# Kernel tuning notes

Measured on AMD Instinct MI355X. Metric: run time of the kernel, lower is better.

## Reference

```python
import jax, jax.numpy as jnp
import numpy as np

WINDOW = (2, 6, 12)  # (Wz, Wh, Ww), N = 144
HEADS = 6
TYPE_OF_WINDOWS = 10


def _position_index(ws):
    Wz, Wh, Ww = ws
    zi = np.arange(Wz); zj = -np.arange(Wz) * Wz
    hi = np.arange(Wh); hj = -np.arange(Wh) * Wh
    w = np.arange(Ww)
    c1 = np.stack(np.meshgrid(zi, hi, w, indexing='ij')).reshape(3, -1)
    c2 = np.stack(np.meshgrid(zj, hj, w, indexing='ij')).reshape(3, -1)
    coords = (c1[:, :, None] - c2[:, None, :]).transpose(1, 2, 0).copy()
    coords[:, :, 2] += Ww - 1
    coords[:, :, 1] *= 2 * Ww - 1
    coords[:, :, 0] *= (2 * Ww - 1) * Wh * Wh
    return coords.sum(-1).reshape(-1)  # [N*N]


def setup_inputs() -> dict:
    key = jax.random.key(0)
    ks = jax.random.split(key, 7)
    B, nW, C = 96, TYPE_OF_WINDOWS, 192
    N = WINDOW[0] * WINDOW[1] * WINDOW[2]
    bias_len = (2 * WINDOW[2] - 1) * WINDOW[1] ** 2 * WINDOW[0] ** 2
    return {
        'x': jax.random.normal(ks[0], (B, nW, N, C), jnp.float32),
        'mask': jax.random.normal(ks[1], (B, N, N), jnp.float32),
        'w_qkv': jax.random.normal(ks[2], (C, 3 * C), jnp.float32) * 0.02,
        'b_qkv': jnp.zeros((3 * C,), jnp.float32),
        'w_proj': jax.random.normal(ks[3], (C, C), jnp.float32) * 0.02,
        'b_proj': jnp.zeros((C,), jnp.float32),
        'bias_table': jax.random.normal(ks[4], (bias_len, nW, HEADS), jnp.float32) * 0.02,
        'position_index': jnp.asarray(_position_index(WINDOW), jnp.int32),
    }


def reference(x, mask, w_qkv, b_qkv, w_proj, b_proj, bias_table, position_index):
    B, nW, N, C = x.shape
    H = HEADS
    Dh = C // H
    scale = Dh ** -0.5
    qkv = x @ w_qkv + b_qkv                       # [B,nW,N,3C]
    qkv = qkv.reshape(B, nW, N, 3, H, Dh)
    qkv = qkv.transpose(3, 0, 1, 4, 2, 5)         # [3,B,nW,H,N,Dh]
    q, k, v = qkv[0], qkv[1], qkv[2]
    attn = jnp.einsum('bwhnd,bwhmd->bwhnm', q * scale, k)   # [B,nW,H,N,N]
    bias = bias_table[position_index]             # [N*N,nW,H]
    bias = bias.reshape(N, N, nW, H).transpose(2, 3, 0, 1)  # [nW,H,N,N]
    attn = attn + bias[None] + mask[:, None, None, :, :]
    attn = jax.nn.softmax(attn, axis=-1)
    out = jnp.einsum('bwhnm,bwhmd->bwhnd', attn, v)         # [B,nW,H,N,Dh]
    out = out.transpose(0, 1, 3, 2, 4).reshape(B, nW, N, C)
    return out @ w_proj + b_proj
```

## Files before the change

kernel.cpp:

```cpp
#include <hip/hip_runtime.h>
#include <math.h>

#define B_   96
#define NW   10
#define NN   144
#define CC   192
#define HH   6
#define DH   32
#define SCALE 0.17677669529663687f

#define XP 200
#define PP 152
#define NPASS 3
#define BWCHUNK 320
#define QKV_STRIDE (NN * DH)

typedef __attribute__((ext_vector_type(8))) short v8s;
typedef __attribute__((ext_vector_type(4))) unsigned short v4us;
typedef __attribute__((ext_vector_type(4))) float v4f;

__device__ __forceinline__ unsigned short f2b(float f) {
  union { float f; unsigned u; } v; v.f = f;
  unsigned r = v.u + 0x7fffu + ((v.u >> 16) & 1u);
  return (unsigned short)(r >> 16);
}
__device__ __forceinline__ float b2f(unsigned short s) {
  union { unsigned u; float f; } v; v.u = ((unsigned)s) << 16;
  return v.f;
}

#define N_WQT (576*192)
#define N_WPT (192*192)
#define N_BIAS (NW*HH*NN*NN)

__global__ __launch_bounds__(256) void prep_kernel(
    const float* __restrict__ w_qkv, const float* __restrict__ w_proj,
    const float* __restrict__ bias_table, const int* __restrict__ pos,
    unsigned short* __restrict__ wqT, unsigned short* __restrict__ wpT,
    unsigned short* __restrict__ biasNN)
{
  int i = blockIdx.x * 256 + threadIdx.x;
  if (i < N_WQT) {
    int n = i / 192, k = i % 192;
    wqT[i] = f2b(w_qkv[k * 576 + n]);
  } else if (i < N_WQT + N_WPT) {
    int j = i - N_WQT;
    int n = j / 192, k = j % 192;
    wpT[j] = f2b(w_proj[k * 192 + n]);
  } else if (i < N_WQT + N_WPT + N_BIAS) {
    int j = i - (N_WQT + N_WPT);
    int m = j % NN, n = (j / NN) % NN, h = (j / (NN * NN)) % HH, w = j / (NN * NN * HH);
    biasNN[j] = f2b(bias_table[(pos[n * NN + m] * NW + w) * HH + h]);
  }
}

__global__ __launch_bounds__(256, 3) void qkv_gemm(
    const float* __restrict__ x, const float* __restrict__ b_qkv,
    const unsigned short* __restrict__ wqT,
    unsigned short* __restrict__ qkv, int bw0)
{
  __shared__ unsigned short xs[48 * XP];
  const int tid  = threadIdx.x;
  const int wave = tid >> 6, lane = tid & 63;
  const int lr = lane & 15, lk8 = (lane >> 4) * 8, quad = lane >> 4;
  const int bwl = blockIdx.x / 3;
  const int rt3 = blockIdx.x % 3;
  const int bw  = bw0 + bwl;

  const float4* xp4 = (const float4*)(x + ((size_t)bw * NN + rt3 * 48) * CC);
  for (int i = tid; i < 48 * (CC / 4); i += 256) {
    float4 f = xp4[i];
    int r = i / (CC / 4), c = (i % (CC / 4)) * 4;
    unsigned short* d = &xs[r * XP + c];
    d[0] = f2b(f.x); d[1] = f2b(f.y); d[2] = f2b(f.z); d[3] = f2b(f.w);
  }
  __syncthreads();

  v8s a[3][6];
  #pragma unroll
  for (int ii = 0; ii < 3; ii++)
    #pragma unroll
    for (int ks = 0; ks < 6; ks++)
      a[ii][ks] = *(const v8s*)&xs[(ii * 16 + lr) * XP + ks * 32 + lk8];

  for (int c = wave; c < 36; c += 4) {
    const int s = c / 12;
    const int h = (c % 12) >> 1;
    const int dhalf = c & 1;
    const unsigned short* wrow = wqT + (size_t)(c * 16 + lr) * CC;
    v8s bf[6];
    #pragma unroll
    for (int ks = 0; ks < 6; ks++) bf[ks] = *(const v8s*)&wrow[ks * 32 + lk8];
    const float bv = b_qkv[c * 16 + lr];
    v4f acc[3];
    #pragma unroll
    for (int ii = 0; ii < 3; ii++) acc[ii] = (v4f){bv, bv, bv, bv};
    #pragma unroll
    for (int ks = 0; ks < 6; ks++)
      #pragma unroll
      for (int ii = 0; ii < 3; ii++)
        acc[ii] = __builtin_amdgcn_mfma_f32_16x16x32_bf16(a[ii][ks], bf[ks], acc[ii], 0, 0, 0);

    if (s == 2) {
      unsigned short* opT = qkv + ((size_t)(bwl * HH + h) * 3 + 2) * QKV_STRIDE
                          + (size_t)(dhalf * 16 + lr) * NN;
      #pragma unroll
      for (int ii = 0; ii < 3; ii++) {
        const int n0 = rt3 * 48 + ii * 16 + quad * 4;
        v4us pk;
        #pragma unroll
        for (int r = 0; r < 4; r++) pk[r] = f2b(acc[ii][r]);
        *(v4us*)&opT[n0] = pk;
      }
    } else {
      unsigned short* op = qkv + ((size_t)(bwl * HH + h) * 3 + s) * QKV_STRIDE + dhalf * 16 + lr;
      #pragma unroll
      for (int ii = 0; ii < 3; ii++)
        #pragma unroll
        for (int r = 0; r < 4; r++) {
          const int n = rt3 * 48 + ii * 16 + quad * 4 + r;
          op[n * DH] = f2b(acc[ii][r]);
        }
    }
  }
}

__global__ __launch_bounds__(256, 2) void attn_bwh(
    const unsigned short* __restrict__ qkv, const float* __restrict__ mask,
    const unsigned short* __restrict__ biasNN,
    unsigned short* __restrict__ ao, int bw0)
{
  __shared__ unsigned short Ps[NN * PP];

  const int tid  = threadIdx.x;
  const int wave = tid >> 6, lane = tid & 63;
  const int lr = lane & 15, lk8 = (lane >> 4) * 8, quad = lane >> 4;

  const int bwl = blockIdx.x / HH;
  const int h   = blockIdx.x % HH;
  const int bw  = bw0 + bwl;
  const int b   = bw / NW;
  const int w   = bw % NW;

  const unsigned short* qp = qkv + (size_t)(bwl * HH + h) * 3 * QKV_STRIDE;
  const unsigned short* kp = qp + QKV_STRIDE;
  const unsigned short* vT = qp + 2 * QKV_STRIDE;

  v8s bv[2][4], bvt[2];
  #pragma unroll
  for (int dh2 = 0; dh2 < 2; dh2++) {
    const unsigned short* vrow = vT + (size_t)(dh2 * 16 + lr) * NN;
    #pragma unroll
    for (int ks = 0; ks < 4; ks++) bv[dh2][ks] = *(const v8s*)&vrow[ks * 32 + lk8];
    bvt[dh2] = *(const v8s*)&vrow[128 + (lk8 & 8)];
  }

  v8s aq[9];
  #pragma unroll
  for (int nt = 0; nt < 9; nt++)
    aq[nt] = *(const v8s*)&qp[(nt * 16 + lr) * DH + lk8];

  for (int mt = wave; mt < 9; mt += 4) {
    v8s bk = *(const v8s*)&kp[(mt * 16 + lr) * DH + lk8];
    const int m = mt * 16 + lr;
    #pragma unroll
    for (int nt = 0; nt < 9; nt++) {
      v4f c = {0.f, 0.f, 0.f, 0.f};
      c = __builtin_amdgcn_mfma_f32_16x16x32_bf16(aq[nt], bk, c, 0, 0, 0);
      #pragma unroll
      for (int r = 0; r < 4; r++) {
        const int n = nt * 16 + quad * 4 + r;
        Ps[n * PP + m] = f2b(c[r] * SCALE);
      }
    }
  }
  __syncthreads();

  const unsigned short* bp = biasNN + (size_t)(w * HH + h) * NN * NN;
  const float* mp = mask + (size_t)b * NN * NN;
  for (int rr = 0; rr < 9; rr++) {
    const int row = rr * 16 + wave * 4 + quad;
    unsigned short* prow = &Ps[row * PP];
    const unsigned short* brow = bp + (size_t)row * NN;
    const float* mrow = mp + (size_t)row * NN;
    float bm[9];
    #pragma unroll
    for (int j = 0; j < 9; j++)
      bm[j] = b2f(brow[j * 16 + lr]) + mrow[j * 16 + lr];
    float e[9];
    float mx = -1e30f;
    #pragma unroll
    for (int j = 0; j < 9; j++) {
      e[j] = b2f(prow[j * 16 + lr]) + bm[j];
      mx = fmaxf(mx, e[j]);
    }
    #pragma unroll
    for (int off = 8; off; off >>= 1) mx = fmaxf(mx, __shfl_xor(mx, off, 64));
    float s = 0.f;
    #pragma unroll
    for (int j = 0; j < 9; j++) { e[j] = __expf(e[j] - mx); s += e[j]; }
    #pragma unroll
    for (int off = 8; off; off >>= 1) s += __shfl_xor(s, off, 64);
    const float inv = 1.f / s;
    #pragma unroll
    for (int j = 0; j < 9; j++) prow[j * 16 + lr] = f2b(e[j] * inv);
  }
  __syncthreads();

  const v8s vzero = {};
  for (int nt = wave; nt < 9; nt += 4) {
    v8s ap[4];
    #pragma unroll
    for (int ks = 0; ks < 4; ks++)
      ap[ks] = *(const v8s*)&Ps[(nt * 16 + lr) * PP + ks * 32 + lk8];
    v8s at = *(const v8s*)&Ps[(nt * 16 + lr) * PP + 128 + (lk8 & 8)];
    at = (quad < 2) ? at : vzero;
    #pragma unroll
    for (int dh2 = 0; dh2 < 2; dh2++) {
      v4f c = {0.f, 0.f, 0.f, 0.f};
      #pragma unroll
      for (int ks = 0; ks < 4; ks++)
        c = __builtin_amdgcn_mfma_f32_16x16x32_bf16(ap[ks], bv[dh2][ks], c, 0, 0, 0);
      c = __builtin_amdgcn_mfma_f32_16x16x32_bf16(at, bvt[dh2], c, 0, 0, 0);
      #pragma unroll
      for (int r = 0; r < 4; r++) {
        const int n = nt * 16 + quad * 4 + r;
        ao[((size_t)bw * NN + n) * CC + h * DH + dh2 * 16 + lr] = f2b(c[r]);
      }
    }
  }
}

__global__ __launch_bounds__(256) void proj_mfma(
    const unsigned short* __restrict__ ao,
    const unsigned short* __restrict__ wpT,
    const float* __restrict__ b_proj,
    float* __restrict__ out)
{
  const int tid  = threadIdx.x;
  const int wave = tid >> 6, lane = tid & 63;
  const int lr = lane & 15, lk8 = (lane >> 4) * 8, quad = lane >> 4;
  const size_t row0 = (size_t)blockIdx.x * 64;
  const int j0 = wave * 3;

  v8s bf[3][6];
  #pragma unroll
  for (int jj = 0; jj < 3; jj++)
    #pragma unroll
    for (int ks = 0; ks < 6; ks++)
      bf[jj][ks] = *(const v8s*)(wpT + (size_t)((j0 + jj) * 16 + lr) * CC + ks * 32 + lk8);

  float bvj[3];
  #pragma unroll
  for (int jj = 0; jj < 3; jj++) bvj[jj] = b_proj[(j0 + jj) * 16 + lr];

  #pragma unroll
  for (int rt = 0; rt < 4; rt++) {
    const size_t r0 = row0 + rt * 16;
    v8s a[6];
    #pragma unroll
    for (int ks = 0; ks < 6; ks++)
      a[ks] = *(const v8s*)(ao + (r0 + lr) * CC + ks * 32 + lk8);
    v4f acc[3];
    #pragma unroll
    for (int jj = 0; jj < 3; jj++) acc[jj] = (v4f){bvj[jj], bvj[jj], bvj[jj], bvj[jj]};
    #pragma unroll
    for (int ks = 0; ks < 6; ks++)
      #pragma unroll
      for (int jj = 0; jj < 3; jj++)
        acc[jj] = __builtin_amdgcn_mfma_f32_16x16x32_bf16(a[ks], bf[jj][ks], acc[jj], 0, 0, 0);
    #pragma unroll
    for (int jj = 0; jj < 3; jj++)
      #pragma unroll
      for (int r = 0; r < 4; r++)
        out[(r0 + quad * 4 + r) * CC + (j0 + jj) * 16 + lr] = acc[jj][r];
  }
}

extern "C" void kernel_launch(void* const* d_in, const int* in_sizes, int n_in,
                              void* d_out, int out_size, void* d_ws, size_t ws_size,
                              hipStream_t stream)
{
  const float* x          = (const float*)d_in[0];
  const float* mask       = (const float*)d_in[1];
  const float* w_qkv      = (const float*)d_in[2];
  const float* b_qkv      = (const float*)d_in[3];
  const float* w_proj     = (const float*)d_in[4];
  const float* b_proj     = (const float*)d_in[5];
  const float* bias_table = (const float*)d_in[6];
  const int*   pos        = (const int*)d_in[7];
  float* out = (float*)d_out;

  unsigned short* biasNN = (unsigned short*)d_ws;
  unsigned short* wqT    = biasNN + N_BIAS;
  unsigned short* wpT    = wqT + N_WQT;
  unsigned short* qkvws  = wpT + N_WPT;
  unsigned short* ao     = qkvws + (size_t)BWCHUNK * HH * 3 * QKV_STRIDE;

  const int prep_total = N_WQT + N_WPT + N_BIAS;
  prep_kernel<<<(prep_total + 255) / 256, 256, 0, stream>>>(
      w_qkv, w_proj, bias_table, pos, wqT, wpT, biasNN);

  for (int p = 0; p < NPASS; p++) {
    const int bw0 = p * BWCHUNK;
    qkv_gemm<<<BWCHUNK * 3, 256, 0, stream>>>(x, b_qkv, wqT, qkvws, bw0);
    attn_bwh<<<BWCHUNK * HH, 256, 0, stream>>>(qkvws, mask, biasNN, ao, bw0);
  }
  proj_mfma<<<(B_ * NW * NN) / 64, 256, 0, stream>>>(ao, wpT, b_proj, out);
}
```

Measured before the change: 476.1 us.

## Fuse QKV projection into attention kernel with per-head LDS staging

```diff
diff --git a/kernel.cpp b/kernel.cpp
--- a/kernel.cpp
+++ b/kernel.cpp
@@ -9,11 +9,10 @@
 #define DH   32
 #define SCALE 0.17677669529663687f
 
-#define XP 200
+#define QP 40
+#define TP 168
 #define PP 152
-#define NPASS 3
-#define BWCHUNK 320
-#define QKV_STRIDE (NN * DH)
+#define NBW (B_ * NW)
 
 typedef __attribute__((ext_vector_type(8))) short v8s;
 typedef __attribute__((ext_vector_type(4))) unsigned short v4us;
@@ -32,14 +31,24 @@
 #define N_WQT (576*192)
 #define N_WPT (192*192)
 #define N_BIAS (NW*HH*NN*NN)
+#define N_X4  (B_*NW*NN*CC/4)
 
 __global__ __launch_bounds__(256) void prep_kernel(
     const float* __restrict__ w_qkv, const float* __restrict__ w_proj,
     const float* __restrict__ bias_table, const int* __restrict__ pos,
+    const float* __restrict__ x,
     unsigned short* __restrict__ wqT, unsigned short* __restrict__ wpT,
-    unsigned short* __restrict__ biasNN)
+    unsigned short* __restrict__ biasNN, unsigned short* __restrict__ xb)
 {
   int i = blockIdx.x * 256 + threadIdx.x;
+  if (i < N_X4) {
+    float4 f = ((const float4*)x)[i];
+    v4us pk;
+    pk[0] = f2b(f.x); pk[1] = f2b(f.y); pk[2] = f2b(f.z); pk[3] = f2b(f.w);
+    *(v4us*)&xb[i * 4] = pk;
+    return;
+  }
+  i -= N_X4;
   if (i < N_WQT) {
     int n = i / 192, k = i % 192;
     wqT[i] = f2b(w_qkv[k * 576 + n]);
@@ -54,102 +63,62 @@
   }
 }
 
-__global__ __launch_bounds__(256, 3) void qkv_gemm(
-    const float* __restrict__ x, const float* __restrict__ b_qkv,
-    const unsigned short* __restrict__ wqT,
-    unsigned short* __restrict__ qkv, int bw0)
-{
-  __shared__ unsigned short xs[48 * XP];
+__global__ __launch_bounds__(256, 2) void fused_attn(
+    const unsigned short* __restrict__ xb, const float* __restrict__ b_qkv,
+    const unsigned short* __restrict__ wqT, const float* __restrict__ mask,
+    const unsigned short* __restrict__ biasNN,
+    unsigned short* __restrict__ ao)
+{
+  __shared__ unsigned short q_lds[NN * QP];
+  __shared__ unsigned short k_lds[NN * QP];
+  __shared__ unsigned short vT[DH * TP];
+  __shared__ unsigned short Ps[NN * PP];
+
   const int tid  = threadIdx.x;
   const int wave = tid >> 6, lane = tid & 63;
   const int lr = lane & 15, lk8 = (lane >> 4) * 8, quad = lane >> 4;
-  const int bwl = blockIdx.x / 3;
-  const int rt3 = blockIdx.x % 3;
-  const int bw  = bw0 + bwl;
-
-  const float4* xp4 = (const float4*)(x + ((size_t)bw * NN + rt3 * 48) * CC);
-  for (int i = tid; i < 48 * (CC / 4); i += 256) {
-    float4 f = xp4[i];
-    int r = i / (CC / 4), c = (i % (CC / 4)) * 4;
-    unsigned short* d = &xs[r * XP + c];
-    d[0] = f2b(f.x); d[1] = f2b(f.y); d[2] = f2b(f.z); d[3] = f2b(f.w);
+
+  const int bw = blockIdx.x / HH;
+  const int h  = blockIdx.x % HH;
+  const int b  = bw / NW;
+  const int w  = bw % NW;
+
+  const unsigned short* xrow = xb + (size_t)bw * NN * CC;
+  for (int t = wave; t < 54; t += 4) {
+    const int nt = t / 6, c = t % 6;
+    const int s = c >> 1, dhalf = c & 1;
+    const int cg = s * 12 + h * 2 + dhalf;
+    v8s a_[6], bf_[6];
+    #pragma unroll
+    for (int ks = 0; ks < 6; ks++)
+      a_[ks] = *(const v8s*)&xrow[(nt * 16 + lr) * CC + ks * 32 + lk8];
+    #pragma unroll
+    for (int ks = 0; ks < 6; ks++)
+      bf_[ks] = *(const v8s*)&wqT[(size_t)(cg * 16 + lr) * CC + ks * 32 + lk8];
+    const float bv0 = b_qkv[cg * 16 + lr];
+    v4f acc = {bv0, bv0, bv0, bv0};
+    #pragma unroll
+    for (int ks = 0; ks < 6; ks++)
+      acc = __builtin_amdgcn_mfma_f32_16x16x32_bf16(a_[ks], bf_[ks], acc, 0, 0, 0);
+    const int d = dhalf * 16 + lr;
+    if (s == 2) {
+      v4us pk;
+      #pragma unroll
+      for (int r = 0; r < 4; r++) pk[r] = f2b(acc[r]);
+      *(v4us*)&vT[d * TP + nt * 16 + quad * 4] = pk;
+    } else {
+      unsigned short* dst = (s == 0) ? q_lds : k_lds;
+      #pragma unroll
+      for (int r = 0; r < 4; r++)
+        dst[(nt * 16 + quad * 4 + r) * QP + d] = f2b(acc[r]);
+    }
   }
   __syncthreads();
 
-  v8s a[3][6];
-  #pragma unroll
-  for (int ii = 0; ii < 3; ii++)
-    #pragma unroll
-    for (int ks = 0; ks < 6; ks++)
-      a[ii][ks] = *(const v8s*)&xs[(ii * 16 + lr) * XP + ks * 32 + lk8];
-
-  for (int c = wave; c < 36; c += 4) {
-    const int s = c / 12;
-    const int h = (c % 12) >> 1;
-    const int dhalf = c & 1;
-    const unsigned short* wrow = wqT + (size_t)(c * 16 + lr) * CC;
-    v8s bf[6];
-    #pragma unroll
-    for (int ks = 0; ks < 6; ks++) bf[ks] = *(const v8s*)&wrow[ks * 32 + lk8];
-    const float bv = b_qkv[c * 16 + lr];
-    v4f acc[3];
-    #pragma unroll
-    for (int ii = 0; ii < 3; ii++) acc[ii] = (v4f){bv, bv, bv, bv};
-    #pragma unroll
-    for (int ks = 0; ks < 6; ks++)
-      #pragma unroll
-      for (int ii = 0; ii < 3; ii++)
-        acc[ii] = __builtin_amdgcn_mfma_f32_16x16x32_bf16(a[ii][ks], bf[ks], acc[ii], 0, 0, 0);
-
-    if (s == 2) {
-      unsigned short* opT = qkv + ((size_t)(bwl * HH + h) * 3 + 2) * QKV_STRIDE
-                          + (size_t)(dhalf * 16 + lr) * NN;
-      #pragma unroll
-      for (int ii = 0; ii < 3; ii++) {
-        const int n0 = rt3 * 48 + ii * 16 + quad * 4;
-        v4us pk;
-        #pragma unroll
-        for (int r = 0; r < 4; r++) pk[r] = f2b(acc[ii][r]);
-        *(v4us*)&opT[n0] = pk;
-      }
-    } else {
-      unsigned short* op = qkv + ((size_t)(bwl * HH + h) * 3 + s) * QKV_STRIDE + dhalf * 16 + lr;
-      #pragma unroll
-      for (int ii = 0; ii < 3; ii++)
-        #pragma unroll
-        for (int r = 0; r < 4; r++) {
-          const int n = rt3 * 48 + ii * 16 + quad * 4 + r;
-          op[n * DH] = f2b(acc[ii][r]);
-        }
-    }
-  }
-}
-
-__global__ __launch_bounds__(256, 2) void attn_bwh(
-    const unsigned short* __restrict__ qkv, const float* __restrict__ mask,
-    const unsigned short* __restrict__ biasNN,
-    unsigned short* __restrict__ ao, int bw0)
-{
-  __shared__ unsigned short Ps[NN * PP];
-
-  const int tid  = threadIdx.x;
-  const int wave = tid >> 6, lane = tid & 63;
-  const int lr = lane & 15, lk8 = (lane >> 4) * 8, quad = lane >> 4;
-
-  const int bwl = blockIdx.x / HH;
-  const int h   = blockIdx.x % HH;
-  const int bw  = bw0 + bwl;
-  const int b   = bw / NW;
-  const int w   = bw % NW;
-
-  const unsigned short* qp = qkv + (size_t)(bwl * HH + h) * 3 * QKV_STRIDE;
-  const unsigned short* kp = qp + QKV_STRIDE;
-  const unsigned short* vT = qp + 2 * QKV_STRIDE;
-
   v8s bv[2][4], bvt[2];
   #pragma unroll
   for (int dh2 = 0; dh2 < 2; dh2++) {
-    const unsigned short* vrow = vT + (size_t)(dh2 * 16 + lr) * NN;
+    const unsigned short* vrow = &vT[(dh2 * 16 + lr) * TP];
     #pragma unroll
     for (int ks = 0; ks < 4; ks++) bv[dh2][ks] = *(const v8s*)&vrow[ks * 32 + lk8];
     bvt[dh2] = *(const v8s*)&vrow[128 + (lk8 & 8)];
@@ -158,10 +127,10 @@
   v8s aq[9];
   #pragma unroll
   for (int nt = 0; nt < 9; nt++)
-    aq[nt] = *(const v8s*)&qp[(nt * 16 + lr) * DH + lk8];
+    aq[nt] = *(const v8s*)&q_lds[(nt * 16 + lr) * QP + lk8];
 
   for (int mt = wave; mt < 9; mt += 4) {
-    v8s bk = *(const v8s*)&kp[(mt * 16 + lr) * DH + lk8];
+    v8s bk = *(const v8s*)&k_lds[(mt * 16 + lr) * QP + lk8];
     const int m = mt * 16 + lr;
     #pragma unroll
     for (int nt = 0; nt < 9; nt++) {
@@ -294,17 +263,14 @@
   unsigned short* biasNN = (unsigned short*)d_ws;
   unsigned short* wqT    = biasNN + N_BIAS;
   unsigned short* wpT    = wqT + N_WQT;
-  unsigned short* qkvws  = wpT + N_WPT;
-  unsigned short* ao     = qkvws + (size_t)BWCHUNK * HH * 3 * QKV_STRIDE;
-
-  const int prep_total = N_WQT + N_WPT + N_BIAS;
+  unsigned short* ao     = wpT + N_WPT;
+  unsigned short* xb     = ao + (size_t)NBW * NN * CC;
+
+  const int prep_total = N_X4 + N_WQT + N_WPT + N_BIAS;
   prep_kernel<<<(prep_total + 255) / 256, 256, 0, stream>>>(
-      w_qkv, w_proj, bias_table, pos, wqT, wpT, biasNN);
-
-  for (int p = 0; p < NPASS; p++) {
-    const int bw0 = p * BWCHUNK;
-    qkv_gemm<<<BWCHUNK * 3, 256, 0, stream>>>(x, b_qkv, wqT, qkvws, bw0);
-    attn_bwh<<<BWCHUNK * HH, 256, 0, stream>>>(qkvws, mask, biasNN, ao, bw0);
-  }
-  proj_mfma<<<(B_ * NW * NN) / 64, 256, 0, stream>>>(ao, wpT, b_proj, out);
-}
+      w_qkv, w_proj, bias_table, pos, x, wqT, wpT, biasNN, xb);
+
+  fused_attn<<<NBW * HH, 256, 0, stream>>>(xb, b_qkv, wqT, mask, biasNN, ao);
+
+  proj_mfma<<<(NBW * NN) / 64, 256, 0, stream>>>(ao, wpT, b_proj, out);
+}
```

After: 761.7 us. 1.6x slower.
